# Optimization experiments

Measured on AMD Instinct MI355X. Metric: run time of the kernel, lower is better.

## Reference

```python
import jax, jax.numpy as jnp
import numpy as np

B, N, C = 16, 1024, 768
E, H, D, K = 8, 192, 4, 2


def setup_inputs() -> dict:
    key = jax.random.key(0)
    ks = jax.random.split(key, 8)
    std = 0.02
    return {
        "x": jax.random.normal(ks[0], (B, N, C), jnp.float32),
        "task_ids": jax.random.randint(ks[1], (B,), 0, D),
        "eps": jax.random.normal(ks[2], (B, N, E), jnp.float32),
        "gate_w": jax.random.normal(ks[3], (D, C, 2 * E), jnp.float32) * std,
        "fc1_w": jax.random.normal(ks[4], (E, H, C), jnp.float32) * std,
        "fc1_b": jnp.zeros((E, H), jnp.float32),
        "fc2_w": jax.random.normal(ks[5], (E, C, H), jnp.float32) * std,
        "fc2_b": jnp.zeros((E, C), jnp.float32),
    }


def reference(x, task_ids, eps, gate_w, fc1_w, fc1_b, fc2_w, fc2_b):
    # per-sample gate selected by domain/task id: [B,N,2E]
    total_w = jnp.einsum("bnc,bce->bne", x, gate_w[task_ids])
    clean_logits, raw_noise = jnp.split(total_w, 2, axis=-1)  # [B,N,E] each
    noise_stddev = jax.nn.softplus(raw_noise) + 0.01
    logits = clean_logits + eps * noise_stddev  # [B,N,E]
    exp_wise_sum = logits.sum(axis=1)  # [B,E]

    top_k_logits, top_k_idx = jax.lax.top_k(exp_wise_sum, K)  # [B,K]
    m1 = top_k_logits.min(axis=1, keepdims=True)
    m2 = top_k_logits.max(axis=1, keepdims=True)
    scaled = (top_k_logits - m1) / (m2 - m1 + 1e-6)
    top_k_gates = jax.nn.softmax(scaled, axis=1)  # [B,K]

    gates_full = jnp.zeros((B, E), x.dtype).at[
        jnp.arange(B)[:, None], top_k_idx
    ].set(top_k_gates)  # [B,E]

    # dense all-expert adapter compute (faithful to original torch.stack)
    h = jnp.einsum("bnc,ehc->benh", x, fc1_w) + fc1_b[None, :, None, :]
    h = jax.nn.gelu(h, approximate=False)
    expert_outs = jnp.einsum("benh,ech->benc", h, fc2_w) + fc2_b[None, :, None, :]

    tot_x = jnp.einsum("be,benc->bnc", gates_full, expert_outs)
    return x + tot_x
```

## Files before the change

kernel.cpp:

```cpp
#include <hip/hip_runtime.h>

#define B_ 16
#define N_ 1024
#define C_ 768
#define E_ 8
#define H_ 192
#define K_ 2

typedef __bf16 bf16x8 __attribute__((ext_vector_type(8)));
typedef float  f32x4  __attribute__((ext_vector_type(4)));

__global__ __launch_bounds__(256) void convert_w_kernel(
    const float* __restrict__ w1, const float* __restrict__ w2,
    __bf16* __restrict__ w1b, __bf16* __restrict__ w2b) {
  int idx = blockIdx.x * 256 + threadIdx.x;
  const int n4 = (E_ * H_ * C_) / 4;
  if (idx >= n4) return;
  float4 a = *(const float4*)(w1 + (size_t)idx * 4);
  float4 b = *(const float4*)(w2 + (size_t)idx * 4);
  __bf16* d1 = w1b + (size_t)idx * 4;
  __bf16* d2 = w2b + (size_t)idx * 4;
  d1[0] = (__bf16)a.x; d1[1] = (__bf16)a.y; d1[2] = (__bf16)a.z; d1[3] = (__bf16)a.w;
  d2[0] = (__bf16)b.x; d2[1] = (__bf16)b.y; d2[2] = (__bf16)b.z; d2[3] = (__bf16)b.w;
}

__global__ __launch_bounds__(256) void gate_kernel(
    const float* __restrict__ x, const int* __restrict__ task_ids,
    const float* __restrict__ eps, const float* __restrict__ gate_w,
    float* __restrict__ sums) {
  const int b = blockIdx.x >> 5;
  const int tile = blockIdx.x & 31;
  const int token0 = tile * 32;
  const int tid = threadIdx.x;

  __shared__ __align__(16) float gwt[16][772];
  __shared__ float sc[16][16];
  __shared__ float red[16][8];

  const int task = task_ids[b];
  const float* gw = gate_w + (size_t)task * C_ * 16;
  for (int it = 0; it < 12; ++it) {
    int idx4 = it * 256 + tid;
    float4 v = *(const float4*)(gw + (size_t)idx4 * 4);
    int flat = idx4 * 4;
    int c = flat >> 4;
    int j = flat & 15;
    gwt[j + 0][c] = v.x; gwt[j + 1][c] = v.y;
    gwt[j + 2][c] = v.z; gwt[j + 3][c] = v.w;
  }
  __syncthreads();

  const int j = tid & 15;
  const int tslot = tid >> 4;
  float part = 0.0f;
  for (int pass = 0; pass < 2; ++pass) {
    const int t = pass * 16 + tslot;
    const int n = token0 + t;
    const float* xr = x + ((size_t)b * N_ + n) * C_;
    float acc = 0.0f;
#pragma unroll 4
    for (int c = 0; c < C_; c += 4) {
      float4 xv = *(const float4*)(xr + c);
      float4 wv = *(const float4*)&gwt[j][c];
      acc += xv.x * wv.x + xv.y * wv.y + xv.z * wv.z + xv.w * wv.w;
    }
    sc[tslot][j] = acc;
    __syncthreads();
    if (j < 8) {
      float clean = sc[tslot][j];
      float raw = sc[tslot][j + 8];
      float sp = (raw > 20.0f) ? raw : log1pf(expf(raw));
      float lg = clean + eps[((size_t)b * N_ + n) * E_ + j] * (sp + 0.01f);
      part += lg;
    }
    __syncthreads();
  }
  if (j < 8) red[tslot][j] = part;
  __syncthreads();
  if (tid < 8) {
    float s = 0.0f;
#pragma unroll
    for (int t = 0; t < 16; ++t) s += red[t][tid];
    atomicAdd(&sums[b * E_ + tid], s);
  }
}

__global__ __launch_bounds__(64) void topk_kernel(
    const float* __restrict__ sums, int* __restrict__ tk_idx,
    float* __restrict__ tk_gate) {
  int tid = threadIdx.x;
  if (tid >= B_) return;
  const float* s = sums + tid * E_;
  float best = -INFINITY, best2 = -INFINITY;
  int i1 = 0, i2 = 0;
#pragma unroll
  for (int e = 0; e < E_; ++e) {
    float v = s[e];
    if (v > best) { best2 = best; i2 = i1; best = v; i1 = e; }
    else if (v > best2) { best2 = v; i2 = e; }
  }
  float d = best - best2;
  float st = d / (d + 1e-6f);
  float et = expf(st);
  tk_idx[tid * 2 + 0] = i1; tk_gate[tid * 2 + 0] = et / (et + 1.0f);
  tk_idx[tid * 2 + 1] = i2; tk_gate[tid * 2 + 1] = 1.0f / (et + 1.0f);
}

__global__ __launch_bounds__(256, 2) void expert_kernel(
    const float* __restrict__ x, const __bf16* __restrict__ w1b,
    const __bf16* __restrict__ w2b, const float* __restrict__ fc1_b,
    const float* __restrict__ fc2_b, const int* __restrict__ tk_idx,
    const float* __restrict__ tk_gate, float* __restrict__ out) {
  const int b = blockIdx.x >> 5;
  const int tile = blockIdx.x & 31;
  const int token0 = tile * 32;
  const int tid = threadIdx.x;
  const int wave = tid >> 6;
  const int lane = tid & 63;
  const int ln = lane & 15;
  const int q8 = (lane >> 4) * 8;
  const int q4 = (lane >> 4) * 4;

  __shared__ __align__(16) __bf16 xs[32][776];
  __shared__ __align__(16) __bf16 hs[32][200];

  int e_idx[2]; float gate_v[2];
  e_idx[0] = tk_idx[b * 2 + 0]; e_idx[1] = tk_idx[b * 2 + 1];
  gate_v[0] = tk_gate[b * 2 + 0]; gate_v[1] = tk_gate[b * 2 + 1];

  const float* xbase = x + ((size_t)b * N_ + token0) * C_;
  for (int it = 0; it < 24; ++it) {
    int chunk = it * 256 + tid;
    int row = chunk / 192;
    int col4 = chunk - row * 192;
    float4 v = *(const float4*)(xbase + (size_t)row * C_ + col4 * 4);
    __bf16* d = &xs[row][col4 * 4];
    d[0] = (__bf16)v.x; d[1] = (__bf16)v.y; d[2] = (__bf16)v.z; d[3] = (__bf16)v.w;
  }
  __syncthreads();

  f32x4 c2[2][12] = {};

  for (int kx = 0; kx < 2; ++kx) {
    const int e = e_idx[kx];
    const float g = gate_v[kx];

    const __bf16* w1p = w1b + (size_t)e * H_ * C_;
    f32x4 c1[2][3] = {};
    for (int k0 = 0; k0 < C_; k0 += 32) {
      bf16x8 a0 = *(const bf16x8*)&xs[ln][k0 + q8];
      bf16x8 a1 = *(const bf16x8*)&xs[16 + ln][k0 + q8];
#pragma unroll
      for (int j = 0; j < 3; ++j) {
        int n = (wave * 3 + j) * 16 + ln;
        bf16x8 bv = *(const bf16x8*)(w1p + (size_t)n * C_ + k0 + q8);
        c1[0][j] = __builtin_amdgcn_mfma_f32_16x16x32_bf16(a0, bv, c1[0][j], 0, 0, 0);
        c1[1][j] = __builtin_amdgcn_mfma_f32_16x16x32_bf16(a1, bv, c1[1][j], 0, 0, 0);
      }
    }
#pragma unroll
    for (int j = 0; j < 3; ++j) {
      int col = (wave * 3 + j) * 16 + ln;
      float b1 = fc1_b[e * H_ + col];
#pragma unroll
      for (int m = 0; m < 2; ++m) {
#pragma unroll
        for (int r = 0; r < 4; ++r) {
          int row = m * 16 + q4 + r;
          float v = c1[m][j][r] + b1;
          float gl = 0.5f * v * (1.0f + erff(v * 0.70710678118f));
          hs[row][col] = (__bf16)(g * gl);
        }
      }
    }
    __syncthreads();

    const __bf16* w2p = w2b + (size_t)e * C_ * H_;
    for (int k0 = 0; k0 < H_; k0 += 32) {
      bf16x8 a0 = *(const bf16x8*)&hs[ln][k0 + q8];
      bf16x8 a1 = *(const bf16x8*)&hs[16 + ln][k0 + q8];
#pragma unroll
      for (int j = 0; j < 12; ++j) {
        int n = (wave * 12 + j) * 16 + ln;
        bf16x8 bv = *(const bf16x8*)(w2p + (size_t)n * H_ + k0 + q8);
        c2[0][j] = __builtin_amdgcn_mfma_f32_16x16x32_bf16(a0, bv, c2[0][j], 0, 0, 0);
        c2[1][j] = __builtin_amdgcn_mfma_f32_16x16x32_bf16(a1, bv, c2[1][j], 0, 0, 0);
      }
    }
    __syncthreads();
  }

  const float* xr = x + ((size_t)b * N_ + token0) * C_;
  float* outr = out + ((size_t)b * N_ + token0) * C_;
#pragma unroll
  for (int j = 0; j < 12; ++j) {
    int col = (wave * 12 + j) * 16 + ln;
    float b2t = gate_v[0] * fc2_b[e_idx[0] * C_ + col] +
                gate_v[1] * fc2_b[e_idx[1] * C_ + col];
#pragma unroll
    for (int m = 0; m < 2; ++m) {
#pragma unroll
      for (int r = 0; r < 4; ++r) {
        int row = m * 16 + q4 + r;
        size_t off = (size_t)row * C_ + col;
        outr[off] = xr[off] + c2[m][j][r] + b2t;
      }
    }
  }
}

extern "C" void kernel_launch(void* const* d_in, const int* in_sizes, int n_in,
                              void* d_out, int out_size, void* d_ws, size_t ws_size,
                              hipStream_t stream) {
  const float* x      = (const float*)d_in[0];
  const int*   task   = (const int*)d_in[1];
  const float* eps    = (const float*)d_in[2];
  const float* gate_w = (const float*)d_in[3];
  const float* fc1_w  = (const float*)d_in[4];
  const float* fc1_b  = (const float*)d_in[5];
  const float* fc2_w  = (const float*)d_in[6];
  const float* fc2_b  = (const float*)d_in[7];
  float* out = (float*)d_out;

  const size_t nW = (size_t)E_ * H_ * C_;
  __bf16* w1b = (__bf16*)d_ws;
  __bf16* w2b = w1b + nW;
  float* sums = (float*)((char*)d_ws + 2 * nW * sizeof(__bf16));
  int* tk_idx = (int*)((char*)sums + 512);
  float* tk_gate = (float*)((char*)tk_idx + 256);

  hipMemsetAsync(sums, 0, B_ * E_ * sizeof(float), stream);
  convert_w_kernel<<<(nW / 4 + 255) / 256, 256, 0, stream>>>(fc1_w, fc2_w, w1b, w2b);
  gate_kernel<<<B_ * 32, 256, 0, stream>>>(x, task, eps, gate_w, sums);
  topk_kernel<<<1, 64, 0, stream>>>(sums, tk_idx, tk_gate);
  expert_kernel<<<B_ * 32, 256, 0, stream>>>(x, w1b, w2b, fc1_b, fc2_b,
                                             tk_idx, tk_gate, out);
}
```

Baseline: 243.0 us.

## Pre-pack expert weights into MFMA tile layout, double-buffer loads, fold topk into expert kernel

The weight conversion kernel now writes fc1/fc2 weights in a k-block-major packed layout so each wave's MFMA B-operand loads are contiguous, and it also transposes the gate weights. The expert kernel double-buffers weight and activation fragments across k-steps to overlap global loads with MFMA work, computes top-k inline (dropping the topk kernel launch), and vectorizes the x-to-bf16 staging stores. The gate kernel is restructured to stage x tiles of 16 tokens in LDS and read gate weights from global, doubling its block count. The extra register use from double buffering could reduce occupancy.

```diff
diff --git a/kernel.cpp b/kernel.cpp
--- a/kernel.cpp
+++ b/kernel.cpp
@@ -10,110 +10,106 @@
 typedef __bf16 bf16x8 __attribute__((ext_vector_type(8)));
 typedef float  f32x4  __attribute__((ext_vector_type(4)));
 
-__global__ __launch_bounds__(256) void convert_w_kernel(
+__global__ __launch_bounds__(256) void prep_kernel(
     const float* __restrict__ w1, const float* __restrict__ w2,
-    __bf16* __restrict__ w1b, __bf16* __restrict__ w2b) {
+    const float* __restrict__ gw,
+    __bf16* __restrict__ pw1, __bf16* __restrict__ pw2,
+    float* __restrict__ gwT) {
   int idx = blockIdx.x * 256 + threadIdx.x;
-  const int n4 = (E_ * H_ * C_) / 4;
-  if (idx >= n4) return;
-  float4 a = *(const float4*)(w1 + (size_t)idx * 4);
-  float4 b = *(const float4*)(w2 + (size_t)idx * 4);
-  __bf16* d1 = w1b + (size_t)idx * 4;
-  __bf16* d2 = w2b + (size_t)idx * 4;
-  d1[0] = (__bf16)a.x; d1[1] = (__bf16)a.y; d1[2] = (__bf16)a.z; d1[3] = (__bf16)a.w;
-  d2[0] = (__bf16)b.x; d2[1] = (__bf16)b.y; d2[2] = (__bf16)b.z; d2[3] = (__bf16)b.w;
-}
-
-__global__ __launch_bounds__(256) void gate_kernel(
+  const int nW4 = (E_ * H_ * C_) / 4;
+  if (idx >= nW4) return;
+  int flat = idx * 4;
+  int e = flat / (H_ * C_);
+  int r = flat - e * (H_ * C_);
+
+  {
+    float4 a = *(const float4*)(w1 + (size_t)flat);
+    int n = r / C_;
+    int c = r - n * C_;
+    size_t o = ((size_t)(e * 24 + (c >> 5)) * 192 + n) * 32 + (c & 31);
+    pw1[o + 0] = (__bf16)a.x; pw1[o + 1] = (__bf16)a.y;
+    pw1[o + 2] = (__bf16)a.z; pw1[o + 3] = (__bf16)a.w;
+  }
+  {
+    float4 a = *(const float4*)(w2 + (size_t)flat);
+    int n = r / H_;
+    int h = r - n * H_;
+    size_t o = ((size_t)(e * 6 + (h >> 5)) * 768 + n) * 32 + (h & 31);
+    pw2[o + 0] = (__bf16)a.x; pw2[o + 1] = (__bf16)a.y;
+    pw2[o + 2] = (__bf16)a.z; pw2[o + 3] = (__bf16)a.w;
+  }
+  if (idx < (4 * 16 * C_) / 4) {
+    int f = idx * 4;
+    int d = f / (16 * C_);
+    int rr = f - d * (16 * C_);
+    int j = rr / C_;
+    int c = rr - j * C_;
+    const float* src = gw + (size_t)d * C_ * 16 + j;
+    float4 v;
+    v.x = src[(size_t)(c + 0) * 16]; v.y = src[(size_t)(c + 1) * 16];
+    v.z = src[(size_t)(c + 2) * 16]; v.w = src[(size_t)(c + 3) * 16];
+    *(float4*)(gwT + (size_t)f) = v;
+  }
+}
+
+__global__ __launch_bounds__(256, 3) void gate_kernel(
     const float* __restrict__ x, const int* __restrict__ task_ids,
-    const float* __restrict__ eps, const float* __restrict__ gate_w,
+    const float* __restrict__ eps, const float* __restrict__ gwT,
     float* __restrict__ sums) {
-  const int b = blockIdx.x >> 5;
-  const int tile = blockIdx.x & 31;
-  const int token0 = tile * 32;
+  const int b = blockIdx.x >> 6;
+  const int token0 = (blockIdx.x & 63) * 16;
   const int tid = threadIdx.x;
 
-  __shared__ __align__(16) float gwt[16][772];
+  __shared__ __align__(16) float xt[16][772];
   __shared__ float sc[16][16];
   __shared__ float red[16][8];
 
+  const float* xbase = x + ((size_t)b * N_ + token0) * C_;
+  for (int it = 0; it < 12; ++it) {
+    int chunk = it * 256 + tid;
+    int row = chunk / 192;
+    int col4 = chunk - row * 192;
+    float4 v = *(const float4*)(xbase + (size_t)row * C_ + col4 * 4);
+    *(float4*)&xt[row][col4 * 4] = v;
+  }
+  __syncthreads();
+
+  const int t = tid & 15;
+  const int j = tid >> 4;
   const int task = task_ids[b];
-  const float* gw = gate_w + (size_t)task * C_ * 16;
-  for (int it = 0; it < 12; ++it) {
-    int idx4 = it * 256 + tid;
-    float4 v = *(const float4*)(gw + (size_t)idx4 * 4);
-    int flat = idx4 * 4;
-    int c = flat >> 4;
-    int j = flat & 15;
-    gwt[j + 0][c] = v.x; gwt[j + 1][c] = v.y;
-    gwt[j + 2][c] = v.z; gwt[j + 3][c] = v.w;
-  }
-  __syncthreads();
-
-  const int j = tid & 15;
-  const int tslot = tid >> 4;
-  float part = 0.0f;
-  for (int pass = 0; pass < 2; ++pass) {
-    const int t = pass * 16 + tslot;
-    const int n = token0 + t;
-    const float* xr = x + ((size_t)b * N_ + n) * C_;
-    float acc = 0.0f;
+  const float* wrow = gwT + ((size_t)task * 16 + j) * C_;
+  float acc = 0.0f;
 #pragma unroll 4
-    for (int c = 0; c < C_; c += 4) {
-      float4 xv = *(const float4*)(xr + c);
-      float4 wv = *(const float4*)&gwt[j][c];
-      acc += xv.x * wv.x + xv.y * wv.y + xv.z * wv.z + xv.w * wv.w;
-    }
-    sc[tslot][j] = acc;
-    __syncthreads();
-    if (j < 8) {
-      float clean = sc[tslot][j];
-      float raw = sc[tslot][j + 8];
-      float sp = (raw > 20.0f) ? raw : log1pf(expf(raw));
-      float lg = clean + eps[((size_t)b * N_ + n) * E_ + j] * (sp + 0.01f);
-      part += lg;
-    }
-    __syncthreads();
-  }
-  if (j < 8) red[tslot][j] = part;
+  for (int c = 0; c < C_; c += 4) {
+    float4 xv = *(const float4*)&xt[t][c];
+    float4 wv = *(const float4*)(wrow + c);
+    acc += xv.x * wv.x + xv.y * wv.y + xv.z * wv.z + xv.w * wv.w;
+  }
+  sc[t][j] = acc;
+  __syncthreads();
+  if (j < 8) {
+    float clean = sc[t][j];
+    float raw = sc[t][j + 8];
+    float sp = (raw > 20.0f) ? raw : log1pf(expf(raw));
+    float lg = clean + eps[((size_t)b * N_ + token0 + t) * E_ + j] * (sp + 0.01f);
+    red[t][j] = lg;
+  }
   __syncthreads();
   if (tid < 8) {
     float s = 0.0f;
 #pragma unroll
-    for (int t = 0; t < 16; ++t) s += red[t][tid];
+    for (int tt = 0; tt < 16; ++tt) s += red[tt][tid];
     atomicAdd(&sums[b * E_ + tid], s);
   }
 }
 
-__global__ __launch_bounds__(64) void topk_kernel(
-    const float* __restrict__ sums, int* __restrict__ tk_idx,
-    float* __restrict__ tk_gate) {
-  int tid = threadIdx.x;
-  if (tid >= B_) return;
-  const float* s = sums + tid * E_;
-  float best = -INFINITY, best2 = -INFINITY;
-  int i1 = 0, i2 = 0;
-#pragma unroll
-  for (int e = 0; e < E_; ++e) {
-    float v = s[e];
-    if (v > best) { best2 = best; i2 = i1; best = v; i1 = e; }
-    else if (v > best2) { best2 = v; i2 = e; }
-  }
-  float d = best - best2;
-  float st = d / (d + 1e-6f);
-  float et = expf(st);
-  tk_idx[tid * 2 + 0] = i1; tk_gate[tid * 2 + 0] = et / (et + 1.0f);
-  tk_idx[tid * 2 + 1] = i2; tk_gate[tid * 2 + 1] = 1.0f / (et + 1.0f);
-}
-
 __global__ __launch_bounds__(256, 2) void expert_kernel(
-    const float* __restrict__ x, const __bf16* __restrict__ w1b,
-    const __bf16* __restrict__ w2b, const float* __restrict__ fc1_b,
-    const float* __restrict__ fc2_b, const int* __restrict__ tk_idx,
-    const float* __restrict__ tk_gate, float* __restrict__ out) {
+    const float* __restrict__ x, const __bf16* __restrict__ pw1,
+    const __bf16* __restrict__ pw2, const float* __restrict__ fc1_b,
+    const float* __restrict__ fc2_b, const float* __restrict__ sums,
+    float* __restrict__ out) {
   const int b = blockIdx.x >> 5;
-  const int tile = blockIdx.x & 31;
-  const int token0 = tile * 32;
+  const int token0 = (blockIdx.x & 31) * 32;
   const int tid = threadIdx.x;
   const int wave = tid >> 6;
   const int lane = tid & 63;
@@ -125,17 +121,35 @@
   __shared__ __align__(16) __bf16 hs[32][200];
 
   int e_idx[2]; float gate_v[2];
-  e_idx[0] = tk_idx[b * 2 + 0]; e_idx[1] = tk_idx[b * 2 + 1];
-  gate_v[0] = tk_gate[b * 2 + 0]; gate_v[1] = tk_gate[b * 2 + 1];
+  {
+    const float* s = sums + b * E_;
+    float best = -INFINITY, best2 = -INFINITY;
+    int i1 = 0, i2 = 0;
+#pragma unroll
+    for (int e = 0; e < E_; ++e) {
+      float v = s[e];
+      if (v > best) { best2 = best; i2 = i1; best = v; i1 = e; }
+      else if (v > best2) { best2 = v; i2 = e; }
+    }
+    float d = best - best2;
+    float st = d / (d + 1e-6f);
+    float et = expf(st);
+    e_idx[0] = i1; gate_v[0] = et / (et + 1.0f);
+    e_idx[1] = i2; gate_v[1] = 1.0f / (et + 1.0f);
+  }
 
   const float* xbase = x + ((size_t)b * N_ + token0) * C_;
-  for (int it = 0; it < 24; ++it) {
+  for (int it = 0; it < 12; ++it) {
     int chunk = it * 256 + tid;
-    int row = chunk / 192;
-    int col4 = chunk - row * 192;
-    float4 v = *(const float4*)(xbase + (size_t)row * C_ + col4 * 4);
-    __bf16* d = &xs[row][col4 * 4];
-    d[0] = (__bf16)v.x; d[1] = (__bf16)v.y; d[2] = (__bf16)v.z; d[3] = (__bf16)v.w;
+    int row = chunk / 96;
+    int col8 = chunk - row * 96;
+    const float* p = xbase + (size_t)row * C_ + col8 * 8;
+    float4 v0 = *(const float4*)p;
+    float4 v1 = *(const float4*)(p + 4);
+    bf16x8 t;
+    t[0] = (__bf16)v0.x; t[1] = (__bf16)v0.y; t[2] = (__bf16)v0.z; t[3] = (__bf16)v0.w;
+    t[4] = (__bf16)v1.x; t[5] = (__bf16)v1.y; t[6] = (__bf16)v1.z; t[7] = (__bf16)v1.w;
+    *(bf16x8*)&xs[row][col8 * 8] = t;
   }
   __syncthreads();
 
@@ -145,22 +159,33 @@
     const int e = e_idx[kx];
     const float g = gate_v[kx];
 
-    const __bf16* w1p = w1b + (size_t)e * H_ * C_;
+    const __bf16* w1l = pw1 + (size_t)e * (24 * 192 * 32)
+                            + (size_t)(wave * 48 + ln) * 32 + q8;
+    bf16x8 bq[2][3], aq[2][2];
+#pragma unroll
+    for (int j = 0; j < 3; ++j) bq[0][j] = *(const bf16x8*)(w1l + j * 512);
+    aq[0][0] = *(const bf16x8*)&xs[ln][q8];
+    aq[0][1] = *(const bf16x8*)&xs[16 + ln][q8];
     f32x4 c1[2][3] = {};
-    for (int k0 = 0; k0 < C_; k0 += 32) {
-      bf16x8 a0 = *(const bf16x8*)&xs[ln][k0 + q8];
-      bf16x8 a1 = *(const bf16x8*)&xs[16 + ln][k0 + q8];
+#pragma unroll
+    for (int kb = 0; kb < 24; ++kb) {
+      int p = kb & 1;
+      if (kb < 23) {
+        const __bf16* nx = w1l + (size_t)(kb + 1) * 6144;
+#pragma unroll
+        for (int j = 0; j < 3; ++j) bq[p ^ 1][j] = *(const bf16x8*)(nx + j * 512);
+        aq[p ^ 1][0] = *(const bf16x8*)&xs[ln][(kb + 1) * 32 + q8];
+        aq[p ^ 1][1] = *(const bf16x8*)&xs[16 + ln][(kb + 1) * 32 + q8];
+      }
 #pragma unroll
       for (int j = 0; j < 3; ++j) {
-        int n = (wave * 3 + j) * 16 + ln;
-        bf16x8 bv = *(const bf16x8*)(w1p + (size_t)n * C_ + k0 + q8);
-        c1[0][j] = __builtin_amdgcn_mfma_f32_16x16x32_bf16(a0, bv, c1[0][j], 0, 0, 0);
-        c1[1][j] = __builtin_amdgcn_mfma_f32_16x16x32_bf16(a1, bv, c1[1][j], 0, 0, 0);
+        c1[0][j] = __builtin_amdgcn_mfma_f32_16x16x32_bf16(aq[p][0], bq[p][j], c1[0][j], 0, 0, 0);
+        c1[1][j] = __builtin_amdgcn_mfma_f32_16x16x32_bf16(aq[p][1], bq[p][j], c1[1][j], 0, 0, 0);
       }
     }
 #pragma unroll
     for (int j = 0; j < 3; ++j) {
-      int col = (wave * 3 + j) * 16 + ln;
+      int col = wave * 48 + j * 16 + ln;
       float b1 = fc1_b[e * H_ + col];
 #pragma unroll
       for (int m = 0; m < 2; ++m) {
@@ -175,16 +200,36 @@
     }
     __syncthreads();
 
-    const __bf16* w2p = w2b + (size_t)e * C_ * H_;
-    for (int k0 = 0; k0 < H_; k0 += 32) {
-      bf16x8 a0 = *(const bf16x8*)&hs[ln][k0 + q8];
-      bf16x8 a1 = *(const bf16x8*)&hs[16 + ln][k0 + q8];
-#pragma unroll
-      for (int j = 0; j < 12; ++j) {
-        int n = (wave * 12 + j) * 16 + ln;
-        bf16x8 bv = *(const bf16x8*)(w2p + (size_t)n * H_ + k0 + q8);
-        c2[0][j] = __builtin_amdgcn_mfma_f32_16x16x32_bf16(a0, bv, c2[0][j], 0, 0, 0);
-        c2[1][j] = __builtin_amdgcn_mfma_f32_16x16x32_bf16(a1, bv, c2[1][j], 0, 0, 0);
+    const __bf16* w2l = pw2 + (size_t)e * (6 * 768 * 32)
+                            + (size_t)(wave * 192 + ln) * 32 + q8;
+    bf16x8 bh[2][6], av[2][2];
+#pragma unroll
+    for (int j = 0; j < 6; ++j) bh[0][j] = *(const bf16x8*)(w2l + j * 512);
+    av[0][0] = *(const bf16x8*)&hs[ln][q8];
+    av[0][1] = *(const bf16x8*)&hs[16 + ln][q8];
+#pragma unroll
+    for (int s = 0; s < 12; ++s) {
+      const int kb = s >> 1;
+      const int half = s & 1;
+      const int p = s & 1;
+      if (s < 11) {
+        const int s2 = s + 1;
+        const int kb2 = s2 >> 1;
+        const int half2 = s2 & 1;
+        const __bf16* src = w2l + (size_t)kb2 * 24576;
+#pragma unroll
+        for (int j = 0; j < 6; ++j)
+          bh[p ^ 1][j] = *(const bf16x8*)(src + (half2 * 6 + j) * 512);
+        if (half2 == 0) {
+          av[kb2 & 1][0] = *(const bf16x8*)&hs[ln][kb2 * 32 + q8];
+          av[kb2 & 1][1] = *(const bf16x8*)&hs[16 + ln][kb2 * 32 + q8];
+        }
+      }
+#pragma unroll
+      for (int j = 0; j < 6; ++j) {
+        const int jj = half * 6 + j;
+        c2[0][jj] = __builtin_amdgcn_mfma_f32_16x16x32_bf16(av[kb & 1][0], bh[p][j], c2[0][jj], 0, 0, 0);
+        c2[1][jj] = __builtin_amdgcn_mfma_f32_16x16x32_bf16(av[kb & 1][1], bh[p][j], c2[1][jj], 0, 0, 0);
       }
     }
     __syncthreads();
@@ -194,7 +239,7 @@
   float* outr = out + ((size_t)b * N_ + token0) * C_;
 #pragma unroll
   for (int j = 0; j < 12; ++j) {
-    int col = (wave * 12 + j) * 16 + ln;
+    int col = wave * 192 + j * 16 + ln;
     float b2t = gate_v[0] * fc2_b[e_idx[0] * C_ + col] +
                 gate_v[1] * fc2_b[e_idx[1] * C_ + col];
 #pragma unroll
@@ -223,16 +268,15 @@
   float* out = (float*)d_out;
 
   const size_t nW = (size_t)E_ * H_ * C_;
-  __bf16* w1b = (__bf16*)d_ws;
-  __bf16* w2b = w1b + nW;
-  float* sums = (float*)((char*)d_ws + 2 * nW * sizeof(__bf16));
-  int* tk_idx = (int*)((char*)sums + 512);
-  float* tk_gate = (float*)((char*)tk_idx + 256);
+  __bf16* pw1 = (__bf16*)d_ws;
+  __bf16* pw2 = pw1 + nW;
+  float* gwT  = (float*)((char*)d_ws + 2 * nW * sizeof(__bf16));
+  float* sums = (float*)((char*)gwT + 4 * 16 * C_ * sizeof(float));
 
   hipMemsetAsync(sums, 0, B_ * E_ * sizeof(float), stream);
-  convert_w_kernel<<<(nW / 4 + 255) / 256, 256, 0, stream>>>(fc1_w, fc2_w, w1b, w2b);
-  gate_kernel<<<B_ * 32, 256, 0, stream>>>(x, task, eps, gate_w, sums);
-  topk_kernel<<<1, 64, 0, stream>>>(sums, tk_idx, tk_gate);
-  expert_kernel<<<B_ * 32, 256, 0, stream>>>(x, w1b, w2b, fc1_b, fc2_b,
-                                             tk_idx, tk_gate, out);
-}
+  prep_kernel<<<(nW / 4 + 255) / 256, 256, 0, stream>>>(fc1_w, fc2_w, gate_w,
+                                                        pw1, pw2, gwT);
+  gate_kernel<<<B_ * 64, 256, 0, stream>>>(x, task, eps, gwT, sums);
+  expert_kernel<<<B_ * 32, 256, 0, stream>>>(x, pw1, pw2, fc1_b, fc2_b,
+                                             sums, out);
+}
```

Result: faster. 209.9 us (-13.7%).
